# Optimization experiments

Hardware: AMD Instinct MI355X
Metric: run time of the kernel (lower is better)

The kernel has to match this reference:

```python
import jax, jax.numpy as jnp
import numpy as np

TEMPERATURE = 10.0
CE_WEIGHT = 10.0
NUM_CLUSTERS = 32  # clusters per batch element, labels in [0, K)


def setup_inputs() -> dict:
    key = jax.random.key(0)
    k1, k2, k3, k4, k5 = jax.random.split(key, 5)
    B, N, D, C, K = 4, 2048, 2, 64, NUM_CLUSTERS
    embedding = jax.random.normal(k1, (B, N, D), dtype=jnp.float32)
    contr_emb = jax.random.normal(k2, (B, N, C), dtype=jnp.float32)
    abs_coords = jax.random.normal(k3, (B, N, D), dtype=jnp.float32)
    patch_mask = jax.random.randint(k4, (B, N, N), 0, 2, dtype=jnp.int32)
    cluster_labels = jax.random.randint(k5, (B, N), 0, K, dtype=jnp.int32)
    return {
        "embedding": embedding,
        "contr_emb": contr_emb,
        "abs_coords": abs_coords,
        "patch_mask": patch_mask,
        "cluster_labels": cluster_labels,
    }


def reference(embedding, contr_emb, abs_coords, patch_mask, cluster_labels):
    B, N, D = embedding.shape
    C = contr_emb.shape[-1]
    K = NUM_CLUSTERS

    # --- anchor term: pairwise distance + nonlinearity + masked mean ---
    # diff[b,i,j,:] = (e_i - e_j) + (c_i - c_j)
    diff = (embedding[:, :, None] - embedding[:, None]) + (
        abs_coords[:, :, None] - abs_coords[:, None]
    )  # [B,N,N,D]
    dist_sq = jnp.sum(diff * diff, axis=-1)  # norm(2)^2, [B,N,N]
    nonlinear_dist = 1.0 - jnp.exp(-dist_sq / TEMPERATURE)
    m = (patch_mask == 1).astype(nonlinear_dist.dtype)
    loss = jnp.sum(nonlinear_dist * m) / jnp.sum(m)  # masked mean

    # --- contrastive term ---
    # F.normalize(contr_emb, dim=-1)
    norm = jnp.maximum(jnp.linalg.norm(contr_emb, axis=-1, keepdims=True), 1e-12)
    c = contr_emb / norm  # [B,N,C]

    # per-batch cluster means under no_grad (stop_gradient)
    onehot = jax.nn.one_hot(cluster_labels, K, dtype=c.dtype)  # [B,N,K]
    sums = jnp.einsum("bnc,bnk->bkc", c, onehot)  # [B,K,C]
    counts = jnp.maximum(jnp.sum(onehot, axis=1), 1.0)  # [B,K]
    means = jax.lax.stop_gradient(sums / counts[..., None])  # [B,K,C]

    # cat per-batch [C,K] matrices along cluster axis -> [C, B*K]
    cum_mean_clusters = means.reshape(B * K, C).T
    stacked = c.reshape(B * N, C)
    logits = stacked @ cum_mean_clusters  # [B*N, B*K]

    target = cluster_labels.reshape(-1)  # labels as written (no batch offset)
    logp = jax.nn.log_softmax(logits, axis=-1)
    nll = -jnp.take_along_axis(logp, target[:, None].astype(jnp.int32), axis=1)[:, 0]
    bce_loss = jnp.mean(nll)  # all targets >= 0, so no ignore_index hits

    return loss + CE_WEIGHT * bce_loss
```

## Files before the change

### kernel.cpp

```cpp
#include <hip/hip_runtime.h>
#include <math.h>

#define B_ 4
#define N_ 2048
#define C_ 64
#define K_ 32
#define BN_ (B_ * N_)

#define WS_NLL 0
#define WS_DONE 8
#define WS_MEANS 64
#define WS_APART 8320

__device__ __forceinline__ void proc4(int4 m, float rx, float ry,
                                      float4 xs, float4 ys,
                                      float& S, int& cnt) {
  float dx, dy, d2;
  dx = rx - xs.x; dy = ry - ys.x; d2 = dx * dx + dy * dy;
  S += (float)m.x * __expf(d2 * -0.1f); cnt += m.x;
  dx = rx - xs.y; dy = ry - ys.y; d2 = dx * dx + dy * dy;
  S += (float)m.y * __expf(d2 * -0.1f); cnt += m.y;
  dx = rx - xs.z; dy = ry - ys.z; d2 = dx * dx + dy * dy;
  S += (float)m.z * __expf(d2 * -0.1f); cnt += m.z;
  dx = rx - xs.w; dy = ry - ys.w; d2 = dx * dx + dy * dy;
  S += (float)m.w * __expf(d2 * -0.1f); cnt += m.w;
}

__global__ __launch_bounds__(256) void k_main(
    const float* __restrict__ emb, const float* __restrict__ absc,
    const float* __restrict__ contr, const int* __restrict__ labels,
    const int* __restrict__ mask, float* __restrict__ ws) {
  __shared__ union {
    struct { float sx[N_]; float sy[N_]; } a;
    struct { int lab[N_]; float lsum[4][64]; float lcnt[4]; } c;
  } sm;
  __shared__ float red[8];
  int t = threadIdx.x, lane = t & 63, w = t >> 6;
  int bid = blockIdx.x;
  if (bid < 128) {
    int b = bid >> 5, k = bid & 31;
    if (bid == 0 && t == 0) {
      ws[WS_NLL] = 0.0f;
      ((unsigned*)ws)[WS_DONE] = 0u;
    }
    const int4* lab4 = (const int4*)(labels + b * N_);
    int4* l4 = (int4*)sm.c.lab;
    l4[t] = lab4[t];
    l4[t + 256] = lab4[t + 256];
    __syncthreads();
    float acc = 0.0f, cnt = 0.0f;
    for (int g0 = w * 512; g0 < w * 512 + 512; g0 += 64) {
      unsigned long long mb = __ballot(sm.c.lab[g0 + lane] == k);
      while (mb) {
        int bit = __ffsll(mb) - 1;
        mb &= mb - 1;
        int r = g0 + bit;
        float x = contr[(size_t)(b * N_ + r) * C_ + lane];
        float ss = x * x;
#pragma unroll
        for (int off = 32; off > 0; off >>= 1) ss += __shfl_xor(ss, off);
        acc += x * (1.0f / fmaxf(sqrtf(ss), 1e-12f));
        cnt += 1.0f;
      }
    }
    sm.c.lsum[w][lane] = acc;
    if (lane == 0) sm.c.lcnt[w] = cnt;
    __syncthreads();
    if (t < 64) {
      float s = sm.c.lsum[0][t] + sm.c.lsum[1][t] + sm.c.lsum[2][t] + sm.c.lsum[3][t];
      float c = sm.c.lcnt[0] + sm.c.lcnt[1] + sm.c.lcnt[2] + sm.c.lcnt[3];
      ws[WS_MEANS + (b * K_ + k) * C_ + t] = s / fmaxf(c, 1.0f);
    }
  } else {
    int aid = bid - 128;
    int b = aid >> 8;
    int aid8 = aid & 255;
    const float4* e4 = (const float4*)(emb + b * N_ * 2);
    const float4* a4 = (const float4*)(absc + b * N_ * 2);
    for (int i = t; i < N_ / 2; i += 256) {
      float4 ev = e4[i], av = a4[i];
      sm.a.sx[2 * i]     = ev.x + av.x;
      sm.a.sy[2 * i]     = ev.y + av.y;
      sm.a.sx[2 * i + 1] = ev.z + av.z;
      sm.a.sy[2 * i + 1] = ev.w + av.w;
    }
    __syncthreads();
    int cg = (aid8 & 1) * 256 + t;
    float4 xs = ((const float4*)sm.a.sx)[cg];
    float4 ys = ((const float4*)sm.a.sy)[cg];
    int rb0 = aid8 >> 1;
    const int4* mp = (const int4*)mask + (size_t)b * (N_ * (size_t)N_ / 4)
                     + aid8 * 256 + t;
    int4 c0 = mp[0], c1 = mp[65536], c2 = mp[131072], c3 = mp[196608];
    float S = 0.0f;
    int cnt = 0;
#pragma unroll 1
    for (int g = 0; g < 3; ++g) {
      const int4* np = mp + (size_t)(g + 1) * 262144;
      int4 n0 = np[0], n1 = np[65536], n2 = np[131072], n3 = np[196608];
      int rr = rb0 + g * 512;
      proc4(c0, sm.a.sx[rr],       sm.a.sy[rr],       xs, ys, S, cnt);
      proc4(c1, sm.a.sx[rr + 128], sm.a.sy[rr + 128], xs, ys, S, cnt);
      proc4(c2, sm.a.sx[rr + 256], sm.a.sy[rr + 256], xs, ys, S, cnt);
      proc4(c3, sm.a.sx[rr + 384], sm.a.sy[rr + 384], xs, ys, S, cnt);
      c0 = n0; c1 = n1; c2 = n2; c3 = n3;
    }
    int rr = rb0 + 3 * 512;
    proc4(c0, sm.a.sx[rr],       sm.a.sy[rr],       xs, ys, S, cnt);
    proc4(c1, sm.a.sx[rr + 128], sm.a.sy[rr + 128], xs, ys, S, cnt);
    proc4(c2, sm.a.sx[rr + 256], sm.a.sy[rr + 256], xs, ys, S, cnt);
    proc4(c3, sm.a.sx[rr + 384], sm.a.sy[rr + 384], xs, ys, S, cnt);
    float cntf = (float)cnt;
    float acc = cntf - S;
#pragma unroll
    for (int off = 32; off > 0; off >>= 1) {
      acc += __shfl_xor(acc, off);
      cntf += __shfl_xor(cntf, off);
    }
    if (lane == 0) { red[w * 2] = acc; red[w * 2 + 1] = cntf; }
    __syncthreads();
    if (t == 0) {
      ws[WS_APART + aid * 2 + 0] = red[0] + red[2] + red[4] + red[6];
      ws[WS_APART + aid * 2 + 1] = red[1] + red[3] + red[5] + red[7];
    }
  }
}

__global__ __launch_bounds__(128) void k_logits_final(
    const float* __restrict__ contr, const int* __restrict__ labels,
    float* __restrict__ ws, float* __restrict__ out) {
  __shared__ float lc[16 * C_];
  __shared__ float invr[16];
  __shared__ float lsv[2][16], ltl[16];
  __shared__ float fred[4];
  __shared__ int lastf;
  int t = threadIdx.x, lane = t & 63, w = t >> 6;
  int r0 = blockIdx.x * 16;
  int j = w * 64 + lane;
  const float4* mean4 = (const float4*)(ws + WS_MEANS);
  float4 mk[16];
#pragma unroll
  for (int q = 0; q < 16; ++q) mk[q] = mean4[j * 16 + q];
  const float4* c4 = (const float4*)(contr + (size_t)r0 * C_);
  float4* lc4 = (float4*)lc;
  lc4[t] = c4[t];
  lc4[t + 128] = c4[t + 128];
  __syncthreads();
  if (t < 16) {
    float ss = 0.0f;
#pragma unroll
    for (int q = 0; q < 16; ++q) {
      float4 v = lc4[t * 16 + q];
      ss += v.x * v.x + v.y * v.y + v.z * v.z + v.w * v.w;
    }
    invr[t] = 1.0f / fmaxf(sqrtf(ss), 1e-12f);
  }
  __syncthreads();
#pragma unroll 1
  for (int rg = 0; rg < 4; ++rg) {
    const float4* cr = lc4 + rg * 64;
    float a0 = 0.0f, a1 = 0.0f, a2 = 0.0f, a3 = 0.0f;
#pragma unroll
    for (int q = 0; q < 16; ++q) {
      float4 m = mk[q];
      float4 cc0 = cr[q], cc1 = cr[16 + q], cc2 = cr[32 + q], cc3 = cr[48 + q];
      a0 += cc0.x * m.x + cc0.y * m.y + cc0.z * m.z + cc0.w * m.w;
      a1 += cc1.x * m.x + cc1.y * m.y + cc1.z * m.z + cc1.w * m.w;
      a2 += cc2.x * m.x + cc2.y * m.y + cc2.z * m.z + cc2.w * m.w;
      a3 += cc3.x * m.x + cc3.y * m.y + cc3.z * m.z + cc3.w * m.w;
    }
    int rb = rg * 4;
    float l0 = a0 * invr[rb + 0];
    float l1 = a1 * invr[rb + 1];
    float l2 = a2 * invr[rb + 2];
    float l3 = a3 * invr[rb + 3];
    float s0 = __expf(l0), s1 = __expf(l1), s2 = __expf(l2), s3 = __expf(l3);
#pragma unroll
    for (int off = 32; off > 0; off >>= 1) {
      s0 += __shfl_xor(s0, off);
      s1 += __shfl_xor(s1, off);
      s2 += __shfl_xor(s2, off);
      s3 += __shfl_xor(s3, off);
    }
    int tg0 = labels[r0 + rb + 0], tg1 = labels[r0 + rb + 1];
    int tg2 = labels[r0 + rb + 2], tg3 = labels[r0 + rb + 3];
    float t0 = __shfl(l0, tg0), t1 = __shfl(l1, tg1);
    float t2 = __shfl(l2, tg2), t3 = __shfl(l3, tg3);
    if (lane == 0) {
      lsv[w][rb + 0] = s0; lsv[w][rb + 1] = s1;
      lsv[w][rb + 2] = s2; lsv[w][rb + 3] = s3;
      if (w == 0) { ltl[rb] = t0; ltl[rb + 1] = t1; ltl[rb + 2] = t2; ltl[rb + 3] = t3; }
    }
  }
  __syncthreads();
  if (t < 16) {
    float nll = __logf(lsv[0][t] + lsv[1][t]) - ltl[t];
#pragma unroll
    for (int off = 8; off > 0; off >>= 1) nll += __shfl_xor(nll, off);
    if (t == 0) atomicAdd(&ws[WS_NLL], nll);
  }
  __syncthreads();
  if (t == 0) {
    __threadfence();
    unsigned v = atomicAdd(&((unsigned*)ws)[WS_DONE], 1u);
    lastf = (v == 511u);
  }
  __syncthreads();
  if (lastf) {
    __threadfence();
    float a = 0.0f, c = 0.0f;
    for (int i = t; i < 1024; i += 128) {
      a += ws[WS_APART + i * 2 + 0];
      c += ws[WS_APART + i * 2 + 1];
    }
#pragma unroll
    for (int off = 32; off > 0; off >>= 1) {
      a += __shfl_xor(a, off);
      c += __shfl_xor(c, off);
    }
    if (lane == 0) { fred[w * 2] = a; fred[w * 2 + 1] = c; }
    __syncthreads();
    if (t == 0) {
      float at = fred[0] + fred[2];
      float ct = fred[1] + fred[3];
      out[0] = at / ct + 10.0f * ws[WS_NLL] * (1.0f / (float)BN_);
    }
  }
}

extern "C" void kernel_launch(void* const* d_in, const int* in_sizes, int n_in,
                              void* d_out, int out_size, void* d_ws, size_t ws_size,
                              hipStream_t stream) {
  const float* emb    = (const float*)d_in[0];
  const float* contr  = (const float*)d_in[1];
  const float* absc   = (const float*)d_in[2];
  const int*   mask   = (const int*)d_in[3];
  const int*   labels = (const int*)d_in[4];
  float* ws  = (float*)d_ws;
  float* out = (float*)d_out;

  k_main<<<128 + 1024, 256, 0, stream>>>(emb, absc, contr, labels, mask, ws);
  k_logits_final<<<512, 128, 0, stream>>>(contr, labels, ws, out);
}
```

Before: 140.5 us.

## Move anchor mask pass into logits kernel to overlap with contrastive work

Splits the work differently across the two launches. The first kernel now only computes cluster means and writes the summed coordinates (embedding plus abs_coords) to the workspace. The second kernel runs the logits/NLL blocks (32 rows each) alongside the heavy mask-streaming anchor blocks, so the mask traffic no longer sits serialized ahead of the logits stage. In exchange, the anchor blocks read row coordinates from global memory instead of LDS, and the last-block completion counter covers both kinds of blocks.

```diff
diff --git a/kernel.cpp b/kernel.cpp
--- a/kernel.cpp
+++ b/kernel.cpp
@@ -11,6 +11,8 @@
 #define WS_DONE 8
 #define WS_MEANS 64
 #define WS_APART 8320
+#define WS_SX 10432
+#define WS_SY 18624
 
 __device__ __forceinline__ void proc4(int4 m, float rx, float ry,
                                       float4 xs, float4 ys,
@@ -26,68 +28,144 @@
   S += (float)m.w * __expf(d2 * -0.1f); cnt += m.w;
 }
 
-__global__ __launch_bounds__(256) void k_main(
+__global__ __launch_bounds__(256) void k_cluster(
     const float* __restrict__ emb, const float* __restrict__ absc,
     const float* __restrict__ contr, const int* __restrict__ labels,
-    const int* __restrict__ mask, float* __restrict__ ws) {
-  __shared__ union {
-    struct { float sx[N_]; float sy[N_]; } a;
-    struct { int lab[N_]; float lsum[4][64]; float lcnt[4]; } c;
-  } sm;
-  __shared__ float red[8];
+    float* __restrict__ ws) {
+  __shared__ int lab[N_];
+  __shared__ float lsum[4][64];
+  __shared__ float lcnt[4];
   int t = threadIdx.x, lane = t & 63, w = t >> 6;
   int bid = blockIdx.x;
-  if (bid < 128) {
-    int b = bid >> 5, k = bid & 31;
-    if (bid == 0 && t == 0) {
-      ws[WS_NLL] = 0.0f;
-      ((unsigned*)ws)[WS_DONE] = 0u;
-    }
-    const int4* lab4 = (const int4*)(labels + b * N_);
-    int4* l4 = (int4*)sm.c.lab;
-    l4[t] = lab4[t];
-    l4[t + 256] = lab4[t + 256];
-    __syncthreads();
-    float acc = 0.0f, cnt = 0.0f;
-    for (int g0 = w * 512; g0 < w * 512 + 512; g0 += 64) {
-      unsigned long long mb = __ballot(sm.c.lab[g0 + lane] == k);
-      while (mb) {
-        int bit = __ffsll(mb) - 1;
-        mb &= mb - 1;
-        int r = g0 + bit;
-        float x = contr[(size_t)(b * N_ + r) * C_ + lane];
-        float ss = x * x;
-#pragma unroll
-        for (int off = 32; off > 0; off >>= 1) ss += __shfl_xor(ss, off);
-        acc += x * (1.0f / fmaxf(sqrtf(ss), 1e-12f));
-        cnt += 1.0f;
-      }
-    }
-    sm.c.lsum[w][lane] = acc;
-    if (lane == 0) sm.c.lcnt[w] = cnt;
-    __syncthreads();
-    if (t < 64) {
-      float s = sm.c.lsum[0][t] + sm.c.lsum[1][t] + sm.c.lsum[2][t] + sm.c.lsum[3][t];
-      float c = sm.c.lcnt[0] + sm.c.lcnt[1] + sm.c.lcnt[2] + sm.c.lcnt[3];
-      ws[WS_MEANS + (b * K_ + k) * C_ + t] = s / fmaxf(c, 1.0f);
+  int b = bid >> 5, k = bid & 31;
+  if (bid == 0 && t == 0) {
+    ws[WS_NLL] = 0.0f;
+    ((unsigned*)ws)[WS_DONE] = 0u;
+  }
+  int flat = bid * 256 + t;
+  if (flat < BN_) {
+    float2 ev = ((const float2*)emb)[flat];
+    float2 av = ((const float2*)absc)[flat];
+    ws[WS_SX + flat] = ev.x + av.x;
+    ws[WS_SY + flat] = ev.y + av.y;
+  }
+  const int4* lab4 = (const int4*)(labels + b * N_);
+  int4* l4 = (int4*)lab;
+  l4[t] = lab4[t];
+  l4[t + 256] = lab4[t + 256];
+  __syncthreads();
+  float acc = 0.0f, cnt = 0.0f;
+  for (int g0 = w * 512; g0 < w * 512 + 512; g0 += 64) {
+    unsigned long long mb = __ballot(lab[g0 + lane] == k);
+    while (mb) {
+      int bit = __ffsll(mb) - 1;
+      mb &= mb - 1;
+      int r = g0 + bit;
+      float x = contr[(size_t)(b * N_ + r) * C_ + lane];
+      float ss = x * x;
+#pragma unroll
+      for (int off = 32; off > 0; off >>= 1) ss += __shfl_xor(ss, off);
+      acc += x * (1.0f / fmaxf(sqrtf(ss), 1e-12f));
+      cnt += 1.0f;
+    }
+  }
+  lsum[w][lane] = acc;
+  if (lane == 0) lcnt[w] = cnt;
+  __syncthreads();
+  if (t < 64) {
+    float s = lsum[0][t] + lsum[1][t] + lsum[2][t] + lsum[3][t];
+    float c = lcnt[0] + lcnt[1] + lcnt[2] + lcnt[3];
+    ws[WS_MEANS + (b * K_ + k) * C_ + t] = s / fmaxf(c, 1.0f);
+  }
+}
+
+__global__ __launch_bounds__(256) void k_fused(
+    const float* __restrict__ contr, const int* __restrict__ labels,
+    const int* __restrict__ mask, float* __restrict__ ws,
+    float* __restrict__ out) {
+  __shared__ float lc[32 * C_];
+  __shared__ float invr[32];
+  __shared__ float lsv[2][32], ltl[32];
+  __shared__ float red[8];
+  __shared__ float fred[8];
+  __shared__ int lastf;
+  int t = threadIdx.x, lane = t & 63, w = t >> 6;
+  int bid = blockIdx.x;
+  if (bid < 256) {
+    int r0 = bid * 32;
+    int ch = w & 1, rh = w >> 1;
+    int j = ch * 64 + lane;
+    const float4* mean4 = (const float4*)(ws + WS_MEANS);
+    float4 mk[16];
+#pragma unroll
+    for (int q = 0; q < 16; ++q) mk[q] = mean4[j * 16 + q];
+    const float4* c4 = (const float4*)(contr + (size_t)r0 * C_);
+    float4* lc4 = (float4*)lc;
+    lc4[t] = c4[t];
+    lc4[t + 256] = c4[t + 256];
+    __syncthreads();
+    if (t < 32) {
+      float ss = 0.0f;
+#pragma unroll
+      for (int q = 0; q < 16; ++q) {
+        float4 v = lc4[t * 16 + q];
+        ss += v.x * v.x + v.y * v.y + v.z * v.z + v.w * v.w;
+      }
+      invr[t] = 1.0f / fmaxf(sqrtf(ss), 1e-12f);
+    }
+    __syncthreads();
+#pragma unroll 1
+    for (int rg = 0; rg < 4; ++rg) {
+      int rb = rh * 16 + rg * 4;
+      const float4* cr = lc4 + rb * 16;
+      float a0 = 0.0f, a1 = 0.0f, a2 = 0.0f, a3 = 0.0f;
+#pragma unroll
+      for (int q = 0; q < 16; ++q) {
+        float4 m = mk[q];
+        float4 c0 = cr[q], c1 = cr[16 + q], c2 = cr[32 + q], c3 = cr[48 + q];
+        a0 += c0.x * m.x + c0.y * m.y + c0.z * m.z + c0.w * m.w;
+        a1 += c1.x * m.x + c1.y * m.y + c1.z * m.z + c1.w * m.w;
+        a2 += c2.x * m.x + c2.y * m.y + c2.z * m.z + c2.w * m.w;
+        a3 += c3.x * m.x + c3.y * m.y + c3.z * m.z + c3.w * m.w;
+      }
+      float l0 = a0 * invr[rb + 0];
+      float l1 = a1 * invr[rb + 1];
+      float l2 = a2 * invr[rb + 2];
+      float l3 = a3 * invr[rb + 3];
+      float s0 = __expf(l0), s1 = __expf(l1), s2 = __expf(l2), s3 = __expf(l3);
+#pragma unroll
+      for (int off = 32; off > 0; off >>= 1) {
+        s0 += __shfl_xor(s0, off);
+        s1 += __shfl_xor(s1, off);
+        s2 += __shfl_xor(s2, off);
+        s3 += __shfl_xor(s3, off);
+      }
+      int tg0 = labels[r0 + rb + 0], tg1 = labels[r0 + rb + 1];
+      int tg2 = labels[r0 + rb + 2], tg3 = labels[r0 + rb + 3];
+      float t0 = __shfl(l0, tg0), t1 = __shfl(l1, tg1);
+      float t2 = __shfl(l2, tg2), t3 = __shfl(l3, tg3);
+      if (lane == 0) {
+        lsv[ch][rb + 0] = s0; lsv[ch][rb + 1] = s1;
+        lsv[ch][rb + 2] = s2; lsv[ch][rb + 3] = s3;
+        if (ch == 0) { ltl[rb] = t0; ltl[rb + 1] = t1; ltl[rb + 2] = t2; ltl[rb + 3] = t3; }
+      }
+    }
+    __syncthreads();
+    if (t < 32) {
+      float nll = __logf(lsv[0][t] + lsv[1][t]) - ltl[t];
+#pragma unroll
+      for (int off = 16; off > 0; off >>= 1) nll += __shfl_xor(nll, off);
+      if (t == 0) atomicAdd(&ws[WS_NLL], nll);
     }
   } else {
-    int aid = bid - 128;
+    int aid = bid - 256;
     int b = aid >> 8;
     int aid8 = aid & 255;
-    const float4* e4 = (const float4*)(emb + b * N_ * 2);
-    const float4* a4 = (const float4*)(absc + b * N_ * 2);
-    for (int i = t; i < N_ / 2; i += 256) {
-      float4 ev = e4[i], av = a4[i];
-      sm.a.sx[2 * i]     = ev.x + av.x;
-      sm.a.sy[2 * i]     = ev.y + av.y;
-      sm.a.sx[2 * i + 1] = ev.z + av.z;
-      sm.a.sy[2 * i + 1] = ev.w + av.w;
-    }
-    __syncthreads();
+    const float* sxp = ws + WS_SX + b * N_;
+    const float* syp = ws + WS_SY + b * N_;
     int cg = (aid8 & 1) * 256 + t;
-    float4 xs = ((const float4*)sm.a.sx)[cg];
-    float4 ys = ((const float4*)sm.a.sy)[cg];
+    float4 xs = ((const float4*)sxp)[cg];
+    float4 ys = ((const float4*)syp)[cg];
     int rb0 = aid8 >> 1;
     const int4* mp = (const int4*)mask + (size_t)b * (N_ * (size_t)N_ / 4)
                      + aid8 * 256 + t;
@@ -99,17 +177,17 @@
       const int4* np = mp + (size_t)(g + 1) * 262144;
       int4 n0 = np[0], n1 = np[65536], n2 = np[131072], n3 = np[196608];
       int rr = rb0 + g * 512;
-      proc4(c0, sm.a.sx[rr],       sm.a.sy[rr],       xs, ys, S, cnt);
-      proc4(c1, sm.a.sx[rr + 128], sm.a.sy[rr + 128], xs, ys, S, cnt);
-      proc4(c2, sm.a.sx[rr + 256], sm.a.sy[rr + 256], xs, ys, S, cnt);
-      proc4(c3, sm.a.sx[rr + 384], sm.a.sy[rr + 384], xs, ys, S, cnt);
+      proc4(c0, sxp[rr],       syp[rr],       xs, ys, S, cnt);
+      proc4(c1, sxp[rr + 128], syp[rr + 128], xs, ys, S, cnt);
+      proc4(c2, sxp[rr + 256], syp[rr + 256], xs, ys, S, cnt);
+      proc4(c3, sxp[rr + 384], syp[rr + 384], xs, ys, S, cnt);
       c0 = n0; c1 = n1; c2 = n2; c3 = n3;
     }
     int rr = rb0 + 3 * 512;
-    proc4(c0, sm.a.sx[rr],       sm.a.sy[rr],       xs, ys, S, cnt);
-    proc4(c1, sm.a.sx[rr + 128], sm.a.sy[rr + 128], xs, ys, S, cnt);
-    proc4(c2, sm.a.sx[rr + 256], sm.a.sy[rr + 256], xs, ys, S, cnt);
-    proc4(c3, sm.a.sx[rr + 384], sm.a.sy[rr + 384], xs, ys, S, cnt);
+    proc4(c0, sxp[rr],       syp[rr],       xs, ys, S, cnt);
+    proc4(c1, sxp[rr + 128], syp[rr + 128], xs, ys, S, cnt);
+    proc4(c2, sxp[rr + 256], syp[rr + 256], xs, ys, S, cnt);
+    proc4(c3, sxp[rr + 384], syp[rr + 384], xs, ys, S, cnt);
     float cntf = (float)cnt;
     float acc = cntf - S;
 #pragma unroll
@@ -124,92 +202,17 @@
       ws[WS_APART + aid * 2 + 1] = red[1] + red[3] + red[5] + red[7];
     }
   }
-}
-
-__global__ __launch_bounds__(128) void k_logits_final(
-    const float* __restrict__ contr, const int* __restrict__ labels,
-    float* __restrict__ ws, float* __restrict__ out) {
-  __shared__ float lc[16 * C_];
-  __shared__ float invr[16];
-  __shared__ float lsv[2][16], ltl[16];
-  __shared__ float fred[4];
-  __shared__ int lastf;
-  int t = threadIdx.x, lane = t & 63, w = t >> 6;
-  int r0 = blockIdx.x * 16;
-  int j = w * 64 + lane;
-  const float4* mean4 = (const float4*)(ws + WS_MEANS);
-  float4 mk[16];
-#pragma unroll
-  for (int q = 0; q < 16; ++q) mk[q] = mean4[j * 16 + q];
-  const float4* c4 = (const float4*)(contr + (size_t)r0 * C_);
-  float4* lc4 = (float4*)lc;
-  lc4[t] = c4[t];
-  lc4[t + 128] = c4[t + 128];
-  __syncthreads();
-  if (t < 16) {
-    float ss = 0.0f;
-#pragma unroll
-    for (int q = 0; q < 16; ++q) {
-      float4 v = lc4[t * 16 + q];
-      ss += v.x * v.x + v.y * v.y + v.z * v.z + v.w * v.w;
-    }
-    invr[t] = 1.0f / fmaxf(sqrtf(ss), 1e-12f);
-  }
-  __syncthreads();
-#pragma unroll 1
-  for (int rg = 0; rg < 4; ++rg) {
-    const float4* cr = lc4 + rg * 64;
-    float a0 = 0.0f, a1 = 0.0f, a2 = 0.0f, a3 = 0.0f;
-#pragma unroll
-    for (int q = 0; q < 16; ++q) {
-      float4 m = mk[q];
-      float4 cc0 = cr[q], cc1 = cr[16 + q], cc2 = cr[32 + q], cc3 = cr[48 + q];
-      a0 += cc0.x * m.x + cc0.y * m.y + cc0.z * m.z + cc0.w * m.w;
-      a1 += cc1.x * m.x + cc1.y * m.y + cc1.z * m.z + cc1.w * m.w;
-      a2 += cc2.x * m.x + cc2.y * m.y + cc2.z * m.z + cc2.w * m.w;
-      a3 += cc3.x * m.x + cc3.y * m.y + cc3.z * m.z + cc3.w * m.w;
-    }
-    int rb = rg * 4;
-    float l0 = a0 * invr[rb + 0];
-    float l1 = a1 * invr[rb + 1];
-    float l2 = a2 * invr[rb + 2];
-    float l3 = a3 * invr[rb + 3];
-    float s0 = __expf(l0), s1 = __expf(l1), s2 = __expf(l2), s3 = __expf(l3);
-#pragma unroll
-    for (int off = 32; off > 0; off >>= 1) {
-      s0 += __shfl_xor(s0, off);
-      s1 += __shfl_xor(s1, off);
-      s2 += __shfl_xor(s2, off);
-      s3 += __shfl_xor(s3, off);
-    }
-    int tg0 = labels[r0 + rb + 0], tg1 = labels[r0 + rb + 1];
-    int tg2 = labels[r0 + rb + 2], tg3 = labels[r0 + rb + 3];
-    float t0 = __shfl(l0, tg0), t1 = __shfl(l1, tg1);
-    float t2 = __shfl(l2, tg2), t3 = __shfl(l3, tg3);
-    if (lane == 0) {
-      lsv[w][rb + 0] = s0; lsv[w][rb + 1] = s1;
-      lsv[w][rb + 2] = s2; lsv[w][rb + 3] = s3;
-      if (w == 0) { ltl[rb] = t0; ltl[rb + 1] = t1; ltl[rb + 2] = t2; ltl[rb + 3] = t3; }
-    }
-  }
-  __syncthreads();
-  if (t < 16) {
-    float nll = __logf(lsv[0][t] + lsv[1][t]) - ltl[t];
-#pragma unroll
-    for (int off = 8; off > 0; off >>= 1) nll += __shfl_xor(nll, off);
-    if (t == 0) atomicAdd(&ws[WS_NLL], nll);
-  }
   __syncthreads();
   if (t == 0) {
     __threadfence();
     unsigned v = atomicAdd(&((unsigned*)ws)[WS_DONE], 1u);
-    lastf = (v == 511u);
+    lastf = (v == 1279u);
   }
   __syncthreads();
   if (lastf) {
     __threadfence();
     float a = 0.0f, c = 0.0f;
-    for (int i = t; i < 1024; i += 128) {
+    for (int i = t; i < 1024; i += 256) {
       a += ws[WS_APART + i * 2 + 0];
       c += ws[WS_APART + i * 2 + 1];
     }
@@ -221,8 +224,8 @@
     if (lane == 0) { fred[w * 2] = a; fred[w * 2 + 1] = c; }
     __syncthreads();
     if (t == 0) {
-      float at = fred[0] + fred[2];
-      float ct = fred[1] + fred[3];
+      float at = fred[0] + fred[2] + fred[4] + fred[6];
+      float ct = fred[1] + fred[3] + fred[5] + fred[7];
       out[0] = at / ct + 10.0f * ws[WS_NLL] * (1.0f / (float)BN_);
     }
   }
@@ -239,6 +242,6 @@
   float* ws  = (float*)d_ws;
   float* out = (float*)d_out;
 
-  k_main<<<128 + 1024, 256, 0, stream>>>(emb, absc, contr, labels, mask, ws);
-  k_logits_final<<<512, 128, 0, stream>>>(contr, labels, ws, out);
-}
+  k_cluster<<<B_ * K_, 256, 0, stream>>>(emb, absc, contr, labels, ws);
+  k_fused<<<256 + 1024, 256, 0, stream>>>(contr, labels, mask, ws, out);
+}
```

Result: slower. 156.0 us (+11.0%).
